# Performance work log

Hardware: AMD Instinct MI355X
Metric: run time of the kernel (lower is better)

## Reference

```python
import jax, jax.numpy as jnp
import numpy as np

DIM = 256
HEADS = 8
HEAD_DIM = DIM // HEADS  # 32
LN_EPS = 1e-5


def setup_inputs() -> dict:
    key = jax.random.key(0)
    ks = jax.random.split(key, 11)
    B, N = 8, 4096
    s = 1.0 / np.sqrt(DIM)
    return {
        "q": jax.random.normal(ks[0], (B, N, DIM), dtype=jnp.float32),
        "k": jax.random.normal(ks[1], (B, N, DIM), dtype=jnp.float32),
        "v": jax.random.normal(ks[2], (B, N, DIM), dtype=jnp.float32),
        "Wq": jax.random.normal(ks[3], (DIM, DIM), dtype=jnp.float32) * s,
        "bq": jax.random.normal(ks[4], (DIM,), dtype=jnp.float32) * 0.01,
        "Wk": jax.random.normal(ks[5], (DIM, DIM), dtype=jnp.float32) * s,
        "bk": jax.random.normal(ks[6], (DIM,), dtype=jnp.float32) * 0.01,
        "Wv": jax.random.normal(ks[7], (DIM, DIM), dtype=jnp.float32) * s,
        "bv": jax.random.normal(ks[8], (DIM,), dtype=jnp.float32) * 0.01,
        "ln_gamma": jnp.ones((DIM,), dtype=jnp.float32),
        "ln_beta": jnp.zeros((DIM,), dtype=jnp.float32),
    }


def _heads(x, B, N):
    # [B, N, DIM] -> [B, HEADS, N, HEAD_DIM]
    return x.reshape(B, N, HEADS, HEAD_DIM).transpose(0, 2, 1, 3)


def reference(q, k, v, Wq, bq, Wk, bk, Wv, bv, ln_gamma, ln_beta):
    B, N, _ = q.shape
    ql = _heads(q @ Wq.T + bq, B, N)
    kl = _heads(k @ Wk.T + bk, B, N)
    vl = _heads(v @ Wv.T + bv, B, N)

    # FFT-domain "attention": rfft2 over (seq, head_dim), complex multiply, irfft2
    q_fft = jnp.fft.rfft2(ql.astype(jnp.float32))   # [B, H, N, HEAD_DIM//2+1] complex
    k_fft = jnp.fft.rfft2(kl.astype(jnp.float32))
    attention = jnp.fft.irfft2(q_fft * k_fft)        # [B, H, N, HEAD_DIM]
    attention = jax.nn.softmax(attention, axis=-1)

    out = vl * attention                             # elementwise value gate
    out = out.transpose(0, 2, 1, 3).reshape(B, N, HEADS * HEAD_DIM)

    # dropout is identity at eval; residual + LayerNorm(256)
    out = out + v
    mu = jnp.mean(out, axis=-1, keepdims=True)
    var = jnp.var(out, axis=-1, keepdims=True)
    out = (out - mu) * jax.lax.rsqrt(var + LN_EPS) * ln_gamma + ln_beta
    return out
```

## Files before the change

### kernel.cpp

```cpp
#include <hip/hip_runtime.h>

#define NFREQ 2049

using cf = float2;
typedef __attribute__((ext_vector_type(8))) short short8;
typedef __attribute__((ext_vector_type(4))) float floatx4;

__device__ inline unsigned short bf16_rne(float x) {
  unsigned u = __float_as_uint(x);
  unsigned r = u + 0x7FFFu + ((u >> 16) & 1u);
  return (unsigned short)(r >> 16);
}
__device__ inline float bf16_to_f(unsigned short h) {
  return __uint_as_float(((unsigned)h) << 16);
}
__device__ inline unsigned pk_bf16(float a, float b) {
  unsigned r;
  asm("v_cvt_pk_bf16_f32 %0, %1, %2" : "=v"(r) : "v"(a), "v"(b));
  return r;
}
__device__ inline cf cmul(cf a, cf b) {
  return make_float2(a.x * b.x - a.y * b.y, a.x * b.y + a.y * b.x);
}
__device__ inline cf cadd(cf a, cf b) { return make_float2(a.x + b.x, a.y + b.y); }
__device__ inline cf csub(cf a, cf b) { return make_float2(a.x - b.x, a.y - b.y); }

__device__ inline void split8(float4 f0, float4 f1, uint4* hi, uint4* lo) {
  unsigned h01 = pk_bf16(f0.x, f0.y), h23 = pk_bf16(f0.z, f0.w);
  unsigned h45 = pk_bf16(f1.x, f1.y), h67 = pk_bf16(f1.z, f1.w);
  float l0 = f0.x - __uint_as_float(h01 << 16);
  float l1 = f0.y - __uint_as_float(h01 & 0xFFFF0000u);
  float l2 = f0.z - __uint_as_float(h23 << 16);
  float l3 = f0.w - __uint_as_float(h23 & 0xFFFF0000u);
  float l4 = f1.x - __uint_as_float(h45 << 16);
  float l5 = f1.y - __uint_as_float(h45 & 0xFFFF0000u);
  float l6 = f1.z - __uint_as_float(h67 << 16);
  float l7 = f1.w - __uint_as_float(h67 & 0xFFFF0000u);
  *hi = make_uint4(h01, h23, h45, h67);
  *lo = make_uint4(pk_bf16(l0, l1), pk_bf16(l2, l3),
                   pk_bf16(l4, l5), pk_bf16(l6, l7));
}

__global__ __launch_bounds__(256) void wconv(
    const float* __restrict__ Wq, const float* __restrict__ Wk,
    const float* __restrict__ Wv,
    unsigned short* __restrict__ Whi, unsigned short* __restrict__ Wlo)
{
  int g = blockIdx.x * 256 + threadIdx.x;
  int c = g & 31, j = (g >> 5) & 255, z = g >> 13;
  const float* W = (z == 0) ? Wq : (z == 1) ? Wk : Wv;
  const float* s = W + (size_t)j * 256 + c * 8;
  uint4 hi, lo;
  split8(*(const float4*)s, *(const float4*)(s + 4), &hi, &lo);
  size_t base = ((size_t)z * 8192 + c * 256 + j) * 8;
  *(uint4*)&Whi[base] = hi;
  *(uint4*)&Wlo[base] = lo;
}

__global__ __launch_bounds__(256, 3) void gemm_proj(
    const float* __restrict__ Xq, const float* __restrict__ bq,
    const float* __restrict__ Xk, const float* __restrict__ bk,
    const float* __restrict__ Xv, const float* __restrict__ bv,
    const unsigned short* __restrict__ Whi, const unsigned short* __restrict__ Wlo,
    float* __restrict__ dq, float* __restrict__ dk, float* __restrict__ dv)
{
  const int z = blockIdx.z;
  const float* X = (z == 0) ? Xq : (z == 1) ? Xk : Xv;
  const float* bias = (z == 0) ? bq : (z == 1) ? bk : bv;
  float* dst = (z == 0) ? dq : (z == 1) ? dk : dv;
  const unsigned short* WhiZ = Whi + (size_t)z * 65536;
  const unsigned short* WloZ = Wlo + (size_t)z * 65536;

  __shared__ __align__(16) unsigned short sm[2][4160];

  const int tid = threadIdx.x;
  const int m0 = blockIdx.x * 64;
  const int wave = tid >> 6, lane = tid & 63;
  const int lm = lane & 15, quad = lane >> 4;

  floatx4 acc[4][4] = {};

  const int srow = tid >> 2, sq = tid & 3;
  const int sIdx = (sq * 65 + srow) << 3;
  const float* aSrc = X + (size_t)(m0 + srow) * 256 + sq * 8;

  int bOff[4];
  #pragma unroll
  for (int jf = 0; jf < 4; jf++) {
    int j = wave * 64 + jf * 16 + lm;
    bOff[jf] = ((quad * 256) + j) << 3;
  }

  {
    uint4 hi, lo;
    split8(*(const float4*)(aSrc), *(const float4*)(aSrc + 4), &hi, &lo);
    *(uint4*)&sm[0][sIdx] = hi;
    *(uint4*)&sm[0][2080 + sIdx] = lo;
  }
  float4 xa0 = *(const float4*)(aSrc + 32);
  float4 xa1 = *(const float4*)(aSrc + 36);
  __syncthreads();

  for (int ks = 0; ks < 8; ks++) {
    const int p = ks & 1;

    short8 bhi[4], blo[4];
    #pragma unroll
    for (int jf = 0; jf < 4; jf++) {
      int off = bOff[jf] + ks * 8192;
      bhi[jf] = *(const short8*)&WhiZ[off];
      blo[jf] = *(const short8*)&WloZ[off];
    }

    short8 ahi[4], alo[4];
    #pragma unroll
    for (int mf = 0; mf < 4; mf++) {
      int idx = (quad * 65 + mf * 16 + lm) << 3;
      ahi[mf] = *(const short8*)&sm[p][idx];
      alo[mf] = *(const short8*)&sm[p][2080 + idx];
    }

    if (ks < 7) {
      uint4 hi, lo;
      split8(xa0, xa1, &hi, &lo);
      *(uint4*)&sm[p ^ 1][sIdx] = hi;
      *(uint4*)&sm[p ^ 1][2080 + sIdx] = lo;
      if (ks < 6) {
        const float* s = aSrc + (ks + 2) * 32;
        xa0 = *(const float4*)s;
        xa1 = *(const float4*)(s + 4);
      }
    }

    #pragma unroll
    for (int mf = 0; mf < 4; mf++)
      #pragma unroll
      for (int jf = 0; jf < 4; jf++) {
        acc[mf][jf] = __builtin_amdgcn_mfma_f32_16x16x32_bf16(
            ahi[mf], bhi[jf], acc[mf][jf], 0, 0, 0);
        acc[mf][jf] = __builtin_amdgcn_mfma_f32_16x16x32_bf16(
            ahi[mf], blo[jf], acc[mf][jf], 0, 0, 0);
        acc[mf][jf] = __builtin_amdgcn_mfma_f32_16x16x32_bf16(
            alo[mf], bhi[jf], acc[mf][jf], 0, 0, 0);
      }

    __syncthreads();
  }

  #pragma unroll
  for (int jf = 0; jf < 4; jf++) {
    float bj = bias[wave * 64 + jf * 16 + lm];
    #pragma unroll
    for (int mf = 0; mf < 4; mf++)
      #pragma unroll
      for (int r = 0; r < 4; r++)
        acc[mf][jf][r] += bj;
  }

  if (z == 2) {
    #pragma unroll
    for (int mf = 0; mf < 4; mf++)
      #pragma unroll
      for (int jf = 0; jf < 4; jf++) {
        int j = wave * 64 + jf * 16 + lm;
        int mb = m0 + mf * 16 + quad * 4;
        #pragma unroll
        for (int r = 0; r < 4; r++)
          dst[(size_t)(mb + r) * 256 + j] = acc[mf][jf][r];
      }
  } else {
    const int b = m0 >> 12;
    const int n0 = m0 & 4095;
    #pragma unroll
    for (int mf = 0; mf < 4; mf++)
      #pragma unroll
      for (int jf = 0; jf < 4; jf++) {
        int j = wave * 64 + jf * 16 + lm;
        int nb = n0 + mf * 16 + quad * 4;
        float4 o = make_float4(acc[mf][jf][0], acc[mf][jf][1],
                               acc[mf][jf][2], acc[mf][jf][3]);
        *(float4*)(dst + (size_t)(b * 256 + j) * 4096 + nb) = o;
      }
  }
}

#define FFT_LDS 4376

__device__ inline int swz(int i) { return i + (i >> 4) + (i >> 8) + (i >> 9); }
__device__ inline int digrev8(int n) {
  return ((n & 7) << 9) | (((n >> 3) & 7) << 6) | (((n >> 6) & 7) << 3) | ((n >> 9) & 7);
}

template<int SIGN>
__device__ inline void fft8_stages(cf* X, int tid)
{
  const float C = 0.70710678118654752f;
  const float sg = (float)SIGN;
  #pragma unroll
  for (int s = 0; s < 4; s++) {
    const int q = 1 << (3 * s);
    __syncthreads();
    #pragma unroll
    for (int r = 0; r < 2; r++) {
      int t = tid + r * 256;
      int j = t & (q - 1);
      int base = ((t >> (3 * s)) << (3 * s + 3)) + j;
      cf x[8];
      #pragma unroll
      for (int l = 0; l < 8; l++) x[l] = X[swz(base + l * q)];
      if (s > 0) {
        float a = sg * 6.283185307179586f * (float)j / (float)(8 * q);
        float sn, cs;
        __sincosf(a, &sn, &cs);
        cf w1 = make_float2(cs, sn);
        cf w = w1;
        #pragma unroll
        for (int l = 1; l < 8; l++) {
          x[l] = cmul(x[l], w);
          if (l < 7) w = cmul(w, w1);
        }
      }
      cf u0 = cadd(x[0], x[4]), v0 = csub(x[0], x[4]);
      cf u1 = cadd(x[1], x[5]), v1 = csub(x[1], x[5]);
      cf u2 = cadd(x[2], x[6]), v2 = csub(x[2], x[6]);
      cf u3 = cadd(x[3], x[7]), v3 = csub(x[3], x[7]);
      cf w1v = make_float2(C * (v1.x - sg * v1.y), C * (v1.y + sg * v1.x));
      cf w2v = make_float2(-sg * v2.y, sg * v2.x);
      cf w3v = make_float2(C * (-v3.x - sg * v3.y), C * (sg * v3.x - v3.y));
      cf e0 = cadd(u0, u2), e1 = csub(u0, u2);
      cf o0 = cadd(u1, u3), o1 = csub(u1, u3);
      cf F0 = cadd(e0, o0), F4 = csub(e0, o0);
      cf F2 = make_float2(e1.x - sg * o1.y, e1.y + sg * o1.x);
      cf F6 = make_float2(e1.x + sg * o1.y, e1.y - sg * o1.x);
      cf e0b = cadd(v0, w2v), e1b = csub(v0, w2v);
      cf o0b = cadd(w1v, w3v), o1b = csub(w1v, w3v);
      cf F1 = cadd(e0b, o0b), F5 = csub(e0b, o0b);
      cf F3 = make_float2(e1b.x - sg * o1b.y, e1b.y + sg * o1b.x);
      cf F7 = make_float2(e1b.x + sg * o1b.y, e1b.y - sg * o1b.x);
      X[swz(base + 0 * q)] = F0;
      X[swz(base + 1 * q)] = F1;
      X[swz(base + 2 * q)] = F2;
      X[swz(base + 3 * q)] = F3;
      X[swz(base + 4 * q)] = F4;
      X[swz(base + 5 * q)] = F5;
      X[swz(base + 6 * q)] = F6;
      X[swz(base + 7 * q)] = F7;
    }
  }
  __syncthreads();
}

__global__ __launch_bounds__(256) void fft_fwd(
    const float* __restrict__ srcQ, cf* __restrict__ dstQ,
    const float* __restrict__ srcK, cf* __restrict__ dstK)
{
  __shared__ cf X[FFT_LDS];
  const float* src_base = blockIdx.y ? srcK : srcQ;
  cf* dst_base = blockIdx.y ? dstK : dstQ;
  const int c0 = blockIdx.x * 2;
  const float* s0 = src_base + (size_t)c0 * 4096;
  const float* s1 = s0 + 4096;
  const int tid = threadIdx.x;
  #pragma unroll
  for (int i = 0; i < 16; i++) {
    int n = tid + i * 256;
    X[swz(digrev8(n))] = make_float2(s0[n], s1[n]);
  }
  fft8_stages<-1>(X, tid);
  cf* d0 = dst_base + (size_t)c0 * NFREQ;
  cf* d1 = d0 + NFREQ;
  for (int f = tid; f <= 2048; f += 256) {
    cf Zf = X[swz(f)];
    cf Zm = X[swz((4096 - f) & 4095)];
    d0[f] = make_float2(0.5f * (Zf.x + Zm.x), 0.5f * (Zf.y - Zm.y));
    d1[f] = make_float2(0.5f * (Zf.y + Zm.y), 0.5f * (Zm.x - Zf.x));
  }
}

__device__ inline cf tw_f(int l, int h) {
  int j = l & (h - 1);
  if (l & h) {
    float sn, cs;
    __sincosf(-3.14159265358979f * (float)j / (float)h, &sn, &cs);
    return make_float2(cs, sn);
  }
  return make_float2(1.0f, 0.0f);
}

template<int H>
__device__ inline cf fwd_stage(cf x, cf w, float sg) {
  float px = __shfl_xor(x.x, H);
  float py = __shfl_xor(x.y, H);
  return cmul(make_float2(px + sg * x.x, py + sg * x.y), w);
}
template<int H>
__device__ inline cf inv_stage(cf x, cf w, float sg) {
  cf t = cmul(x, w);
  float px = __shfl_xor(t.x, H);
  float py = __shfl_xor(t.y, H);
  return make_float2(px + sg * t.x, py + sg * t.y);
}
template<int H>
__device__ inline cf nt_stage(cf x, float sg) {
  float px = __shfl_xor(x.x, H);
  float py = __shfl_xor(x.y, H);
  return make_float2(px + sg * x.x, py + sg * x.y);
}

__global__ __launch_bounds__(256) void freq_conv(
    cf* __restrict__ Qf, const cf* __restrict__ Kf)
{
  __shared__ cf Qs[32][65];
  __shared__ cf Ks[32][65];
  const int f0 = blockIdx.x * 64;
  const int bh = blockIdx.y;
  const int tid = threadIdx.x;
  const int wave = tid >> 6, lane = tid & 63;
  const int d = lane & 31, hl = lane >> 5;

  #pragma unroll
  for (int i = 0; i < 8; i++) {
    int v = tid + i * 256;
    int e = v >> 6, fl = v & 63;
    int f = f0 + fl;
    if (f < NFREQ) {
      Qs[e][fl] = Qf[(size_t)(bh * 32 + e) * NFREQ + f];
      Ks[e][fl] = Kf[(size_t)(bh * 32 + e) * NFREQ + f];
    } else {
      Qs[e][fl] = make_float2(0.0f, 0.0f);
      Ks[e][fl] = make_float2(0.0f, 0.0f);
    }
  }
  __syncthreads();

  const cf w16 = tw_f(d, 16), w8 = tw_f(d, 8), w4 = tw_f(d, 4), w2 = tw_f(d, 2);
  const float s16 = (d & 16) ? -1.0f : 1.0f;
  const float s8  = (d & 8)  ? -1.0f : 1.0f;
  const float s4  = (d & 4)  ? -1.0f : 1.0f;
  const float s2  = (d & 2)  ? -1.0f : 1.0f;
  const float s1  = (d & 1)  ? -1.0f : 1.0f;

  #pragma unroll
  for (int it = 0; it < 8; it++) {
    const int fl = it * 8 + wave * 2 + hl;
    cf q = Qs[d][fl];
    cf k = Ks[d][fl];
    q = fwd_stage<16>(q, w16, s16);  k = fwd_stage<16>(k, w16, s16);
    q = fwd_stage<8>(q, w8, s8);     k = fwd_stage<8>(k, w8, s8);
    q = fwd_stage<4>(q, w4, s4);     k = fwd_stage<4>(k, w4, s4);
    q = fwd_stage<2>(q, w2, s2);     k = fwd_stage<2>(k, w2, s2);
    q = nt_stage<1>(q, s1);          k = nt_stage<1>(k, s1);
    cf c = cmul(q, k);
    c = nt_stage<1>(c, s1);
    c = inv_stage<2>(c, make_float2(w2.x, -w2.y), s2);
    c = inv_stage<4>(c, make_float2(w4.x, -w4.y), s4);
    c = inv_stage<8>(c, make_float2(w8.x, -w8.y), s8);
    c = inv_stage<16>(c, make_float2(w16.x, -w16.y), s16);
    Qs[d][fl] = make_float2(c.x * (1.0f / 32.0f), c.y * (1.0f / 32.0f));
  }
  __syncthreads();

  #pragma unroll
  for (int i = 0; i < 8; i++) {
    int v = tid + i * 256;
    int e = v >> 6, fl = v & 63;
    int f = f0 + fl;
    if (f < NFREQ)
      Qf[(size_t)(bh * 32 + e) * NFREQ + f] = Qs[e][fl];
  }
}

__global__ __launch_bounds__(256) void fft_inv(
    const cf* __restrict__ Cf, float* __restrict__ attn)
{
  __shared__ cf X[FFT_LDS];
  const int c0 = blockIdx.x * 2;
  const cf* s0 = Cf + (size_t)c0 * NFREQ;
  const cf* s1 = s0 + NFREQ;
  const int tid = threadIdx.x;
  for (int f = tid; f <= 2048; f += 256) {
    cf c1 = s0[f];
    cf c2 = s1[f];
    X[swz(digrev8(f))] = make_float2(c1.x - c2.y, c1.y + c2.x);
    if (f != 0 && f != 2048)
      X[swz(digrev8(4096 - f))] = make_float2(c1.x + c2.y, c2.x - c1.y);
  }
  fft8_stages<+1>(X, tid);
  float* d0 = attn + (size_t)c0 * 4096;
  float* d1 = d0 + 4096;
  const float inv = 1.0f / 4096.0f;
  #pragma unroll
  for (int i = 0; i < 16; i++) {
    int n = tid + i * 256;
    cf z = X[swz(n)];
    d0[n] = z.x * inv;
    d1[n] = z.y * inv;
  }
}

__global__ __launch_bounds__(256) void finalize_kernel(
    const float* __restrict__ attn, const float* __restrict__ VL,
    const float* __restrict__ vin, const float* __restrict__ gamma,
    const float* __restrict__ beta, float* __restrict__ out)
{
  __shared__ float At[256][33];
  const int n0 = blockIdx.x * 32;
  const int b = blockIdx.y;
  const int tid = threadIdx.x;
  #pragma unroll
  for (int i = 0; i < 32; i++) {
    int v = tid + i * 256;
    int hd = v >> 5, nn = v & 31;
    At[hd][nn] = attn[(size_t)(b * 256 + hd) * 4096 + n0 + nn];
  }
  __syncthreads();
  const int wave = tid >> 6, lane = tid & 63;
  float g[4], bt[4];
  #pragma unroll
  for (int r = 0; r < 4; r++) { g[r] = gamma[64 * r + lane]; bt[r] = beta[64 * r + lane]; }

  for (int t = 0; t < 8; t++) {
    const int nn = wave * 8 + t;
    const int n = n0 + nn;
    float p[4];
    #pragma unroll
    for (int r = 0; r < 4; r++) {
      float a = At[64 * r + lane][nn];
      float mx = a;
      #pragma unroll
      for (int off = 16; off >= 1; off >>= 1) mx = fmaxf(mx, __shfl_xor(mx, off, 32));
      float e = __expf(a - mx);
      float s = e;
      #pragma unroll
      for (int off = 16; off >= 1; off >>= 1) s += __shfl_xor(s, off, 32);
      p[r] = e / s;
    }
    const size_t base = ((size_t)b * 4096 + n) * 256 + lane;
    float o[4];
    float s1 = 0.0f, s2 = 0.0f;
    #pragma unroll
    for (int r = 0; r < 4; r++) {
      o[r] = VL[base + 64 * r] * p[r] + vin[base + 64 * r];
      s1 += o[r];
      s2 += o[r] * o[r];
    }
    #pragma unroll
    for (int off = 32; off >= 1; off >>= 1) {
      s1 += __shfl_xor(s1, off, 64);
      s2 += __shfl_xor(s2, off, 64);
    }
    float mu = s1 * (1.0f / 256.0f);
    float var = s2 * (1.0f / 256.0f) - mu * mu;
    float rs = rsqrtf(var + 1e-5f);
    #pragma unroll
    for (int r = 0; r < 4; r++)
      out[base + 64 * r] = (o[r] - mu) * rs * g[r] + bt[r];
  }
}

extern "C" void kernel_launch(void* const* d_in, const int* in_sizes, int n_in,
                              void* d_out, int out_size, void* d_ws, size_t ws_size,
                              hipStream_t stream)
{
  const float* q  = (const float*)d_in[0];
  const float* k  = (const float*)d_in[1];
  const float* v  = (const float*)d_in[2];
  const float* Wq = (const float*)d_in[3];
  const float* bq = (const float*)d_in[4];
  const float* Wk = (const float*)d_in[5];
  const float* bk = (const float*)d_in[6];
  const float* Wv = (const float*)d_in[7];
  const float* bv = (const float*)d_in[8];
  const float* ln_gamma = (const float*)d_in[9];
  const float* ln_beta  = (const float*)d_in[10];
  float* out = (float*)d_out;

  float* ws = (float*)d_ws;
  float* QL = ws;
  float* KL = QL + (size_t)8388608;
  float* VL = KL + (size_t)8388608;
  cf* Qf = (cf*)(VL + (size_t)8388608);
  cf* Kf = Qf + (size_t)2048 * NFREQ;
  float* attn = QL;

  unsigned short* Whi = (unsigned short*)Kf;
  unsigned short* Wlo = Whi + (size_t)3 * 65536;

  wconv<<<96, 256, 0, stream>>>(Wq, Wk, Wv, Whi, Wlo);

  gemm_proj<<<dim3(512, 1, 3), 256, 0, stream>>>(q, bq, k, bk, v, bv,
                                                 Whi, Wlo, QL, KL, VL);

  fft_fwd<<<dim3(1024, 2), 256, 0, stream>>>(QL, Qf, KL, Kf);

  freq_conv<<<dim3(33, 64), 256, 0, stream>>>(Qf, Kf);

  fft_inv<<<1024, 256, 0, stream>>>(Qf, attn);

  finalize_kernel<<<dim3(128, 8), 256, 0, stream>>>(attn, VL, v, ln_gamma,
                                                    ln_beta, out);
}
```

Before: 289.9 us.

## Reorder 2D FFT: head-dim DFT first, fused seq-axis convolution, inverse DFT in finalize

Reorders the 2D FFT so the 32-point real DFT over head_dim is computed first as direct matmul-style loops in a dedicated kernel. The 4096-point sequence FFTs, the pointwise product and the inverse FFT are then fused into one complex seqconv kernel per column, and the inverse 32-point DFT moves into the finalize kernel next to softmax and LayerNorm. All projections are now stored row-major, and the separate freq_conv and fft_inv passes are removed. This cuts intermediate global traffic and launches. In exchange it adds direct O(n^2) DFT arithmetic with recurrence twiddles (possible precision drift) and a larger complex workspace.

```diff
diff --git a/kernel.cpp b/kernel.cpp
--- a/kernel.cpp
+++ b/kernel.cpp
@@ -1,19 +1,9 @@
 #include <hip/hip_runtime.h>
-
-#define NFREQ 2049
 
 using cf = float2;
 typedef __attribute__((ext_vector_type(8))) short short8;
 typedef __attribute__((ext_vector_type(4))) float floatx4;
 
-__device__ inline unsigned short bf16_rne(float x) {
-  unsigned u = __float_as_uint(x);
-  unsigned r = u + 0x7FFFu + ((u >> 16) & 1u);
-  return (unsigned short)(r >> 16);
-}
-__device__ inline float bf16_to_f(unsigned short h) {
-  return __uint_as_float(((unsigned)h) << 16);
-}
 __device__ inline unsigned pk_bf16(float a, float b) {
   unsigned r;
   asm("v_cvt_pk_bf16_f32 %0, %1, %2" : "=v"(r) : "v"(a), "v"(b));
@@ -41,6 +31,43 @@
                    pk_bf16(l4, l5), pk_bf16(l6, l7));
 }
 
+__device__ inline void rdft32(const float* x, cf* X) {
+  #pragma unroll
+  for (int k = 0; k <= 16; k++) {
+    float s, c;
+    __sincosf(-3.14159265358979f * (float)k / 16.0f, &s, &c);
+    float wr = 1.0f, wi = 0.0f;
+    float ar = 0.0f, ai = 0.0f;
+    #pragma unroll
+    for (int d = 0; d < 32; d++) {
+      ar += x[d] * wr;
+      ai += x[d] * wi;
+      float t = wr * c - wi * s;
+      wi = wr * s + wi * c;
+      wr = t;
+    }
+    X[k] = make_float2(ar, ai);
+  }
+}
+
+__device__ inline void irdft32(const cf* X, float* x) {
+  #pragma unroll
+  for (int d = 0; d < 32; d++) {
+    float s, c;
+    __sincosf(3.14159265358979f * (float)d / 16.0f, &s, &c);
+    float ur = c, ui = s;
+    float acc = X[0].x + (((d & 1) != 0) ? -X[16].x : X[16].x);
+    #pragma unroll
+    for (int k = 1; k <= 15; k++) {
+      acc += 2.0f * (X[k].x * ur - X[k].y * ui);
+      float t = ur * c - ui * s;
+      ui = ur * s + ui * c;
+      ur = t;
+    }
+    x[d] = acc * 0.03125f;
+  }
+}
+
 __global__ __launch_bounds__(256) void wconv(
     const float* __restrict__ Wq, const float* __restrict__ Wk,
     const float* __restrict__ Wv,
@@ -62,12 +89,12 @@
     const float* __restrict__ Xk, const float* __restrict__ bk,
     const float* __restrict__ Xv, const float* __restrict__ bv,
     const unsigned short* __restrict__ Whi, const unsigned short* __restrict__ Wlo,
-    float* __restrict__ dq, float* __restrict__ dk, float* __restrict__ dv)
+    float* __restrict__ dQm, float* __restrict__ dKm, float* __restrict__ dVm)
 {
   const int z = blockIdx.z;
   const float* X = (z == 0) ? Xq : (z == 1) ? Xk : Xv;
   const float* bias = (z == 0) ? bq : (z == 1) ? bk : bv;
-  float* dst = (z == 0) ? dq : (z == 1) ? dk : dv;
+  float* dst = (z == 0) ? dQm : (z == 1) ? dKm : dVm;
   const unsigned short* WhiZ = Whi + (size_t)z * 65536;
   const unsigned short* WloZ = Wlo + (size_t)z * 65536;
 
@@ -148,40 +175,40 @@
   }
 
   #pragma unroll
-  for (int jf = 0; jf < 4; jf++) {
-    float bj = bias[wave * 64 + jf * 16 + lm];
-    #pragma unroll
-    for (int mf = 0; mf < 4; mf++)
+  for (int mf = 0; mf < 4; mf++)
+    #pragma unroll
+    for (int jf = 0; jf < 4; jf++) {
+      int j = wave * 64 + jf * 16 + lm;
+      float bj = bias[j];
+      int mb = m0 + mf * 16 + quad * 4;
       #pragma unroll
       for (int r = 0; r < 4; r++)
-        acc[mf][jf][r] += bj;
-  }
-
-  if (z == 2) {
-    #pragma unroll
-    for (int mf = 0; mf < 4; mf++)
-      #pragma unroll
-      for (int jf = 0; jf < 4; jf++) {
-        int j = wave * 64 + jf * 16 + lm;
-        int mb = m0 + mf * 16 + quad * 4;
-        #pragma unroll
-        for (int r = 0; r < 4; r++)
-          dst[(size_t)(mb + r) * 256 + j] = acc[mf][jf][r];
-      }
-  } else {
-    const int b = m0 >> 12;
-    const int n0 = m0 & 4095;
-    #pragma unroll
-    for (int mf = 0; mf < 4; mf++)
-      #pragma unroll
-      for (int jf = 0; jf < 4; jf++) {
-        int j = wave * 64 + jf * 16 + lm;
-        int nb = n0 + mf * 16 + quad * 4;
-        float4 o = make_float4(acc[mf][jf][0], acc[mf][jf][1],
-                               acc[mf][jf][2], acc[mf][jf][3]);
-        *(float4*)(dst + (size_t)(b * 256 + j) * 4096 + nb) = o;
-      }
-  }
+        dst[(size_t)(mb + r) * 256 + j] = acc[mf][jf][r] + bj;
+    }
+}
+
+__global__ __launch_bounds__(256) void dfft(
+    const float* __restrict__ src, cf* __restrict__ dst)
+{
+  __shared__ float S[32][257];
+  const int nt = blockIdx.x;
+  const int b = blockIdx.y;
+  const int tid = threadIdx.x;
+  const int n0 = nt * 32;
+  #pragma unroll
+  for (int i = 0; i < 32; i++)
+    S[i][tid] = src[((size_t)(b * 4096 + n0 + i)) * 256 + tid];
+  __syncthreads();
+  const int hh = tid >> 5, row = tid & 31;
+  float xd[32];
+  #pragma unroll
+  for (int d = 0; d < 32; d++) xd[d] = S[row][hh * 32 + d];
+  cf Xo[17];
+  rdft32(xd, Xo);
+  const size_t colbase = ((size_t)(b * 8 + hh) * 17) * 4096 + n0 + row;
+  #pragma unroll
+  for (int fd = 0; fd < 17; fd++)
+    dst[colbase + (size_t)fd * 4096] = Xo[fd];
 }
 
 #define FFT_LDS 4376
@@ -250,211 +277,124 @@
   __syncthreads();
 }
 
-__global__ __launch_bounds__(256) void fft_fwd(
-    const float* __restrict__ srcQ, cf* __restrict__ dstQ,
-    const float* __restrict__ srcK, cf* __restrict__ dstK)
+__global__ __launch_bounds__(256) void seqconv(
+    cf* __restrict__ Qd, const cf* __restrict__ Kd)
 {
   __shared__ cf X[FFT_LDS];
-  const float* src_base = blockIdx.y ? srcK : srcQ;
-  cf* dst_base = blockIdx.y ? dstK : dstQ;
-  const int c0 = blockIdx.x * 2;
-  const float* s0 = src_base + (size_t)c0 * 4096;
-  const float* s1 = s0 + 4096;
+  const size_t cb = (size_t)blockIdx.x * 4096;
   const int tid = threadIdx.x;
+
   #pragma unroll
   for (int i = 0; i < 16; i++) {
     int n = tid + i * 256;
-    X[swz(digrev8(n))] = make_float2(s0[n], s1[n]);
+    X[swz(digrev8(n))] = Qd[cb + n];
   }
   fft8_stages<-1>(X, tid);
-  cf* d0 = dst_base + (size_t)c0 * NFREQ;
-  cf* d1 = d0 + NFREQ;
-  for (int f = tid; f <= 2048; f += 256) {
-    cf Zf = X[swz(f)];
-    cf Zm = X[swz((4096 - f) & 4095)];
-    d0[f] = make_float2(0.5f * (Zf.x + Zm.x), 0.5f * (Zf.y - Zm.y));
-    d1[f] = make_float2(0.5f * (Zf.y + Zm.y), 0.5f * (Zm.x - Zf.x));
-  }
-}
-
-__device__ inline cf tw_f(int l, int h) {
-  int j = l & (h - 1);
-  if (l & h) {
-    float sn, cs;
-    __sincosf(-3.14159265358979f * (float)j / (float)h, &sn, &cs);
-    return make_float2(cs, sn);
-  }
-  return make_float2(1.0f, 0.0f);
-}
-
-template<int H>
-__device__ inline cf fwd_stage(cf x, cf w, float sg) {
-  float px = __shfl_xor(x.x, H);
-  float py = __shfl_xor(x.y, H);
-  return cmul(make_float2(px + sg * x.x, py + sg * x.y), w);
-}
-template<int H>
-__device__ inline cf inv_stage(cf x, cf w, float sg) {
-  cf t = cmul(x, w);
-  float px = __shfl_xor(t.x, H);
-  float py = __shfl_xor(t.y, H);
-  return make_float2(px + sg * t.x, py + sg * t.y);
-}
-template<int H>
-__device__ inline cf nt_stage(cf x, float sg) {
-  float px = __shfl_xor(x.x, H);
-  float py = __shfl_xor(x.y, H);
-  return make_float2(px + sg * x.x, py + sg * x.y);
-}
-
-__global__ __launch_bounds__(256) void freq_conv(
-    cf* __restrict__ Qf, const cf* __restrict__ Kf)
-{
-  __shared__ cf Qs[32][65];
-  __shared__ cf Ks[32][65];
-  const int f0 = blockIdx.x * 64;
-  const int bh = blockIdx.y;
-  const int tid = threadIdx.x;
-  const int wave = tid >> 6, lane = tid & 63;
-  const int d = lane & 31, hl = lane >> 5;
-
-  #pragma unroll
-  for (int i = 0; i < 8; i++) {
-    int v = tid + i * 256;
-    int e = v >> 6, fl = v & 63;
-    int f = f0 + fl;
-    if (f < NFREQ) {
-      Qs[e][fl] = Qf[(size_t)(bh * 32 + e) * NFREQ + f];
-      Ks[e][fl] = Kf[(size_t)(bh * 32 + e) * NFREQ + f];
-    } else {
-      Qs[e][fl] = make_float2(0.0f, 0.0f);
-      Ks[e][fl] = make_float2(0.0f, 0.0f);
-    }
-  }
-  __syncthreads();
-
-  const cf w16 = tw_f(d, 16), w8 = tw_f(d, 8), w4 = tw_f(d, 4), w2 = tw_f(d, 2);
-  const float s16 = (d & 16) ? -1.0f : 1.0f;
-  const float s8  = (d & 8)  ? -1.0f : 1.0f;
-  const float s4  = (d & 4)  ? -1.0f : 1.0f;
-  const float s2  = (d & 2)  ? -1.0f : 1.0f;
-  const float s1  = (d & 1)  ? -1.0f : 1.0f;
-
-  #pragma unroll
-  for (int it = 0; it < 8; it++) {
-    const int fl = it * 8 + wave * 2 + hl;
-    cf q = Qs[d][fl];
-    cf k = Ks[d][fl];
-    q = fwd_stage<16>(q, w16, s16);  k = fwd_stage<16>(k, w16, s16);
-    q = fwd_stage<8>(q, w8, s8);     k = fwd_stage<8>(k, w8, s8);
-    q = fwd_stage<4>(q, w4, s4);     k = fwd_stage<4>(k, w4, s4);
-    q = fwd_stage<2>(q, w2, s2);     k = fwd_stage<2>(k, w2, s2);
-    q = nt_stage<1>(q, s1);          k = nt_stage<1>(k, s1);
-    cf c = cmul(q, k);
-    c = nt_stage<1>(c, s1);
-    c = inv_stage<2>(c, make_float2(w2.x, -w2.y), s2);
-    c = inv_stage<4>(c, make_float2(w4.x, -w4.y), s4);
-    c = inv_stage<8>(c, make_float2(w8.x, -w8.y), s8);
-    c = inv_stage<16>(c, make_float2(w16.x, -w16.y), s16);
-    Qs[d][fl] = make_float2(c.x * (1.0f / 32.0f), c.y * (1.0f / 32.0f));
-  }
-  __syncthreads();
-
-  #pragma unroll
-  for (int i = 0; i < 8; i++) {
-    int v = tid + i * 256;
-    int e = v >> 6, fl = v & 63;
-    int f = f0 + fl;
-    if (f < NFREQ)
-      Qf[(size_t)(bh * 32 + e) * NFREQ + f] = Qs[e][fl];
-  }
-}
-
-__global__ __launch_bounds__(256) void fft_inv(
-    const cf* __restrict__ Cf, float* __restrict__ attn)
-{
-  __shared__ cf X[FFT_LDS];
-  const int c0 = blockIdx.x * 2;
-  const cf* s0 = Cf + (size_t)c0 * NFREQ;
-  const cf* s1 = s0 + NFREQ;
-  const int tid = threadIdx.x;
-  for (int f = tid; f <= 2048; f += 256) {
-    cf c1 = s0[f];
-    cf c2 = s1[f];
-    X[swz(digrev8(f))] = make_float2(c1.x - c2.y, c1.y + c2.x);
-    if (f != 0 && f != 2048)
-      X[swz(digrev8(4096 - f))] = make_float2(c1.x + c2.y, c2.x - c1.y);
-  }
-  fft8_stages<+1>(X, tid);
-  float* d0 = attn + (size_t)c0 * 4096;
-  float* d1 = d0 + 4096;
-  const float inv = 1.0f / 4096.0f;
+
+  cf qs[16];
+  #pragma unroll
+  for (int i = 0; i < 16; i++) qs[i] = X[swz(tid + i * 256)];
+  __syncthreads();
+
   #pragma unroll
   for (int i = 0; i < 16; i++) {
     int n = tid + i * 256;
-    cf z = X[swz(n)];
-    d0[n] = z.x * inv;
-    d1[n] = z.y * inv;
+    X[swz(digrev8(n))] = Kd[cb + n];
+  }
+  fft8_stages<-1>(X, tid);
+
+  const float inv = 1.0f / 4096.0f;
+  #pragma unroll
+  for (int i = 0; i < 16; i++) {
+    cf kv = X[swz(tid + i * 256)];
+    cf p = cmul(qs[i], kv);
+    qs[i] = make_float2(p.x * inv, p.y * inv);
+  }
+  __syncthreads();
+
+  #pragma unroll
+  for (int i = 0; i < 16; i++) {
+    int f = tid + i * 256;
+    X[swz(digrev8(f))] = qs[i];
+  }
+  fft8_stages<+1>(X, tid);
+
+  #pragma unroll
+  for (int i = 0; i < 16; i++) {
+    int n = tid + i * 256;
+    Qd[cb + n] = X[swz(n)];
   }
 }
 
 __global__ __launch_bounds__(256) void finalize_kernel(
-    const float* __restrict__ attn, const float* __restrict__ VL,
+    const cf* __restrict__ Cd, const float* __restrict__ VL,
     const float* __restrict__ vin, const float* __restrict__ gamma,
     const float* __restrict__ beta, float* __restrict__ out)
 {
-  __shared__ float At[256][33];
+  __shared__ cf Cs[136][33];
+  __shared__ float gs[256], bs[256];
   const int n0 = blockIdx.x * 32;
   const int b = blockIdx.y;
   const int tid = threadIdx.x;
-  #pragma unroll
-  for (int i = 0; i < 32; i++) {
-    int v = tid + i * 256;
-    int hd = v >> 5, nn = v & 31;
-    At[hd][nn] = attn[(size_t)(b * 256 + hd) * 4096 + n0 + nn];
-  }
-  __syncthreads();
-  const int wave = tid >> 6, lane = tid & 63;
-  float g[4], bt[4];
-  #pragma unroll
-  for (int r = 0; r < 4; r++) { g[r] = gamma[64 * r + lane]; bt[r] = beta[64 * r + lane]; }
-
-  for (int t = 0; t < 8; t++) {
-    const int nn = wave * 8 + t;
-    const int n = n0 + nn;
-    float p[4];
-    #pragma unroll
-    for (int r = 0; r < 4; r++) {
-      float a = At[64 * r + lane][nn];
-      float mx = a;
-      #pragma unroll
-      for (int off = 16; off >= 1; off >>= 1) mx = fmaxf(mx, __shfl_xor(mx, off, 32));
-      float e = __expf(a - mx);
-      float s = e;
-      #pragma unroll
-      for (int off = 16; off >= 1; off >>= 1) s += __shfl_xor(s, off, 32);
-      p[r] = e / s;
-    }
-    const size_t base = ((size_t)b * 4096 + n) * 256 + lane;
-    float o[4];
-    float s1 = 0.0f, s2 = 0.0f;
-    #pragma unroll
-    for (int r = 0; r < 4; r++) {
-      o[r] = VL[base + 64 * r] * p[r] + vin[base + 64 * r];
-      s1 += o[r];
-      s2 += o[r] * o[r];
-    }
-    #pragma unroll
-    for (int off = 32; off >= 1; off >>= 1) {
-      s1 += __shfl_xor(s1, off, 64);
-      s2 += __shfl_xor(s2, off, 64);
-    }
-    float mu = s1 * (1.0f / 256.0f);
-    float var = s2 * (1.0f / 256.0f) - mu * mu;
-    float rs = rsqrtf(var + 1e-5f);
-    #pragma unroll
-    for (int r = 0; r < 4; r++)
-      out[base + 64 * r] = (o[r] - mu) * rs * g[r] + bt[r];
+  gs[tid] = gamma[tid];
+  bs[tid] = beta[tid];
+  #pragma unroll
+  for (int i = 0; i < 17; i++) {
+    int lin = tid + i * 256;
+    int col = lin >> 5, nl = lin & 31;
+    Cs[col][nl] = Cd[((size_t)b * 136 + col) * 4096 + n0 + nl];
+  }
+  __syncthreads();
+
+  const int h = tid & 7, row = tid >> 3;
+  const int n = n0 + row;
+
+  cf Xs[17];
+  #pragma unroll
+  for (int fd = 0; fd < 17; fd++) Xs[fd] = Cs[h * 17 + fd][row];
+
+  float att[32];
+  irdft32(Xs, att);
+
+  float mx = att[0];
+  #pragma unroll
+  for (int d = 1; d < 32; d++) mx = fmaxf(mx, att[d]);
+  float ssum = 0.f;
+  #pragma unroll
+  for (int d = 0; d < 32; d++) { att[d] = __expf(att[d] - mx); ssum += att[d]; }
+  const float rs = 1.0f / ssum;
+
+  const size_t base = ((size_t)b * 4096 + n) * 256 + h * 32;
+  float o[32];
+  float s1 = 0.f, s2 = 0.f;
+  #pragma unroll
+  for (int i = 0; i < 8; i++) {
+    float4 vl = *(const float4*)(VL + base + i * 4);
+    float4 vi = *(const float4*)(vin + base + i * 4);
+    float o0 = vl.x * (att[i * 4 + 0] * rs) + vi.x;
+    float o1 = vl.y * (att[i * 4 + 1] * rs) + vi.y;
+    float o2 = vl.z * (att[i * 4 + 2] * rs) + vi.z;
+    float o3 = vl.w * (att[i * 4 + 3] * rs) + vi.w;
+    o[i * 4 + 0] = o0; o[i * 4 + 1] = o1; o[i * 4 + 2] = o2; o[i * 4 + 3] = o3;
+    s1 += o0 + o1 + o2 + o3;
+    s2 += o0 * o0 + o1 * o1 + o2 * o2 + o3 * o3;
+  }
+  #pragma unroll
+  for (int off = 1; off < 8; off <<= 1) {
+    s1 += __shfl_xor(s1, off, 64);
+    s2 += __shfl_xor(s2, off, 64);
+  }
+  const float mu = s1 * (1.0f / 256.0f);
+  const float var = s2 * (1.0f / 256.0f) - mu * mu;
+  const float rstd = rsqrtf(var + 1e-5f);
+  #pragma unroll
+  for (int i = 0; i < 8; i++) {
+    float4 ov;
+    ov.x = (o[i * 4 + 0] - mu) * rstd * gs[h * 32 + i * 4 + 0] + bs[h * 32 + i * 4 + 0];
+    ov.y = (o[i * 4 + 1] - mu) * rstd * gs[h * 32 + i * 4 + 1] + bs[h * 32 + i * 4 + 1];
+    ov.z = (o[i * 4 + 2] - mu) * rstd * gs[h * 32 + i * 4 + 2] + bs[h * 32 + i * 4 + 2];
+    ov.w = (o[i * 4 + 3] - mu) * rstd * gs[h * 32 + i * 4 + 3] + bs[h * 32 + i * 4 + 3];
+    *(float4*)(out + base + i * 4) = ov;
   }
 }
 
@@ -476,27 +416,24 @@
   float* out = (float*)d_out;
 
   float* ws = (float*)d_ws;
-  float* QL = ws;
-  float* KL = QL + (size_t)8388608;
-  float* VL = KL + (size_t)8388608;
-  cf* Qf = (cf*)(VL + (size_t)8388608);
-  cf* Kf = Qf + (size_t)2048 * NFREQ;
-  float* attn = QL;
-
-  unsigned short* Whi = (unsigned short*)Kf;
+  float* QLm = ws;
+  cf* Kd = (cf*)ws;
+  float* KLm = ws + (size_t)8912896;
+  float* VL  = ws + (size_t)17301504;
+  cf* Qd = (cf*)(ws + (size_t)25690112);
+  unsigned short* Whi = (unsigned short*)(ws + (size_t)34603008);
   unsigned short* Wlo = Whi + (size_t)3 * 65536;
 
   wconv<<<96, 256, 0, stream>>>(Wq, Wk, Wv, Whi, Wlo);
 
   gemm_proj<<<dim3(512, 1, 3), 256, 0, stream>>>(q, bq, k, bk, v, bv,
-                                                 Whi, Wlo, QL, KL, VL);
-
-  fft_fwd<<<dim3(1024, 2), 256, 0, stream>>>(QL, Qf, KL, Kf);
-
-  freq_conv<<<dim3(33, 64), 256, 0, stream>>>(Qf, Kf);
-
-  fft_inv<<<1024, 256, 0, stream>>>(Qf, attn);
-
-  finalize_kernel<<<dim3(128, 8), 256, 0, stream>>>(attn, VL, v, ln_gamma,
+                                                 Whi, Wlo, QLm, KLm, VL);
+
+  dfft<<<dim3(128, 8), 256, 0, stream>>>(QLm, Qd);
+  dfft<<<dim3(128, 8), 256, 0, stream>>>(KLm, Kd);
+
+  seqconv<<<1088, 256, 0, stream>>>(Qd, Kd);
+
+  finalize_kernel<<<dim3(128, 8), 256, 0, stream>>>(Qd, VL, v, ln_gamma,
                                                     ln_beta, out);
 }
```

Measured after the change: 296.2 us. 2.2% more time.
